# Optimization experiments

Hardware: AMD Instinct MI355X
Metric: run time of the kernel (lower is better)

Reference implementation:

```python
import jax, jax.numpy as jnp
import numpy as np

N = 16384          # nodes
E_R = 524288       # radial edges (avg degree 32)
E_B = 32768        # bonded edges
N_TYPES = 20       # atom types
CS = 64            # scalar (0e) channels
CV = 32            # vector (1o) channels
EA = 16            # edge_attr_dim
EA_B = EA // 2     # bondedness embedding dim
EA_R = (EA + 1) // 2  # radial basis dim
CUTOFF = 1.5       # effective_radial_cutoff
L = 2              # n_layers
NORM = float(np.sqrt((E_R + E_B) / N))  # ~sqrt(avg degree) message normalization


def setup_inputs() -> dict:
    key = jax.random.key(0)
    ks = jax.random.split(key, 32)
    def rn(i, shape, scale=1.0):
        return jax.random.normal(ks[i], shape, dtype=jnp.float32) * scale
    s_e = 1.0 / np.sqrt(EA)
    inp = {}
    inp["pos"] = rn(0, (N, 3))
    inp["c_noise"] = rn(1, (1,))
    inp["atom_types"] = jax.random.randint(ks[2], (N,), 0, N_TYPES)
    inp["radial_edge_index"] = jax.random.randint(ks[3], (2, E_R), 0, N)
    inp["bonded_edge_index"] = jax.random.randint(ks[4], (2, E_B), 0, N)
    # learned parameters
    inp["atom_tab"] = rn(5, (N_TYPES, CS))
    inp["bond_tab"] = rn(6, (2, EA_B))
    inp["ns0_w"] = rn(7, (CS,), 0.1)
    inp["We0"] = rn(8, (EA, CS), s_e)
    inp["We1"] = rn(9, (EA, CS), s_e)
    inp["Wself0"] = rn(10, (CS, CS), 1.0 / np.sqrt(CS))
    inp["Ws0"] = rn(11, (CS, CS), 1.0 / np.sqrt(CS))
    inp["Wv0"] = rn(12, (CS, CV), 1.0 / np.sqrt(CS))
    inp["ns_w"] = rn(13, (L, CS + CV), 0.1)
    inp["We_ss"] = rn(14, (L, EA, CS), s_e)
    inp["We_vs"] = rn(15, (L, EA, CV), s_e)
    inp["We_sv"] = rn(16, (L, EA, CS), s_e)
    inp["We_vv"] = rn(17, (L, EA, CV), s_e)
    inp["We_vx"] = rn(18, (L, EA, CV), s_e)
    inp["Wmix_s"] = rn(19, (L, CS + CV, CS), 1.0 / np.sqrt(CS + CV))
    inp["Wmix_v"] = rn(20, (L, CS + 2 * CV, CV), 1.0 / np.sqrt(CS + 2 * CV))
    inp["Wself_s"] = rn(21, (L, CS, CS), 1.0 / np.sqrt(CS))
    inp["Wself_v"] = rn(22, (L, CV, CV), 1.0 / np.sqrt(CV))
    inp["skip_w"] = rn(23, (L, 2 * (CS + CV)), 0.1)
    inp["skip_b"] = rn(24, (L, 2 * (CS + CV)), 0.1)
    inp["w_out"] = rn(25, (CV,), 1.0 / np.sqrt(CV))
    inp["gain"] = jnp.asarray(0.5, dtype=jnp.float32)
    return inp


def _radial_basis(d):
    # e3nn soft_one_hot_linspace, basis='gaussian', cutoff=True
    centers = jnp.linspace(0.0, CUTOFF, EA_R + 2)[1:-1]
    step = centers[1] - centers[0]
    diff = (d[:, None] - centers[None, :]) / step
    return jnp.exp(-diff * diff) * 1.12


def reference(pos, c_noise, atom_tab, bond_tab, ns0_w, We0, We1, Wself0, Ws0, Wv0,
              ns_w, We_ss, We_vs, We_sv, We_vv, We_vx, Wmix_s, Wmix_v, Wself_s, Wself_v,
              skip_w, skip_b, w_out, gain, atom_types, radial_edge_index, bonded_edge_index):
    edge_index = jnp.concatenate([radial_edge_index, bonded_edge_index], axis=1)
    bond_mask = jnp.concatenate([jnp.zeros((E_R,), jnp.int32), jnp.ones((E_B,), jnp.int32)])
    src, dst = edge_index[0], edge_index[1]
    edge_vec = pos[src] - pos[dst]                      # [E,3]
    d = jnp.sqrt(jnp.sum(edge_vec * edge_vec, -1) + 1e-12)
    Y1 = jnp.sqrt(3.0) * edge_vec / d[:, None]          # l=1 SH, component norm; Y0 == 1
    edge_attr = jnp.concatenate([bond_tab[bond_mask], _radial_basis(d)], axis=-1)  # [E,EA]

    # atom embedding + initial noise-conditional scaling
    s = atom_tab[atom_types] * (1.0 + c_noise * ns0_w)  # [N,CS]

    # initial projector: scalar-input equivariant conv -> hidden irreps
    w0 = edge_attr @ We0
    w1 = edge_attr @ We1
    s_src = s[src]
    a_s = jax.ops.segment_sum(w0 * s_src, dst, num_segments=N) / NORM
    a_v = jax.ops.segment_sum((w1 * s_src)[:, :, None] * Y1[:, None, :], dst, num_segments=N) / NORM
    s_h = a_s @ Ws0 + s @ Wself0                        # [N,CS]
    v_h = jnp.einsum('nci,cd->ndi', a_v, Wv0)           # [N,CV,3]

    for l in range(L):
        # noise-conditional scaling (per-irrep-channel scalar scale)
        scale = 1.0 + c_noise * ns_w[l]
        ss = s_h * scale[:CS]
        vv = v_h * scale[CS:][None, :, None]
        ss_e = ss[src]
        vv_e = vv[src]
        # edge-attr-conditioned tensor-product weights
        w_ss = edge_attr @ We_ss[l]
        w_vs = edge_attr @ We_vs[l]
        w_sv = edge_attr @ We_sv[l]
        w_vv = edge_attr @ We_vv[l]
        w_vx = edge_attr @ We_vx[l]
        # CG tensor-product messages: 0x0->0, 1x1->0 (dot), 0x1->1, 1x0->1, 1x1->1 (cross)
        vdot = jnp.einsum('eci,ei->ec', vv_e, Y1)
        m_s = jnp.concatenate([w_ss * ss_e, w_vs * vdot], axis=-1)          # [E,CS+CV]
        m_v = jnp.concatenate([
            (w_sv * ss_e)[:, :, None] * Y1[:, None, :],
            w_vv[:, :, None] * vv_e,
            w_vx[:, :, None] * jnp.cross(vv_e, Y1[:, None, :]),
        ], axis=1)                                                          # [E,CS+2CV,3]
        a_s = jax.ops.segment_sum(m_s, dst, num_segments=N) / NORM
        a_v = jax.ops.segment_sum(m_v, dst, num_segments=N) / NORM
        new_s = a_s @ Wmix_s[l] + ss @ Wself_s[l]
        new_v = jnp.einsum('nci,cd->ndi', a_v, Wmix_v[l]) + jnp.einsum('nci,cd->ndi', vv, Wself_v[l])
        # noise-conditional skip connection (gated residual)
        g = jax.nn.sigmoid(skip_b[l] + c_noise * skip_w[l])
        s_h = g[:CS] * s_h + g[CS:2 * CS] * new_s
        g_v = g[2 * CS:]
        v_h = g_v[:CV][None, :, None] * v_h + g_v[CV:][None, :, None] * new_v

    # output head: 1o vectors -> 3D displacement, times output gain
    return jnp.einsum('nci,c->ni', v_h, w_out) * gain
```

## Files before the change

kernel.cpp:

```cpp
#include <hip/hip_runtime.h>
#include <math.h>

#define NA 16384
#define ER 524288
#define EB 32768
#define ET 557056
#define INV_NORM 0.17149858514250882f
#define SQRT3 1.7320508075688772f
#define RB_STEP (1.5f/9.0f)
#define BINS 512
#define DMAX 2.5f
#define INV_H ((float)BINS / DMAX)
#define T0U (2 * BINS * 128)
#define TLU (2 * BINS * 256)

typedef unsigned int uint32;
typedef unsigned short ushort16;
typedef float vf4 __attribute__((ext_vector_type(4)));
typedef float vf2 __attribute__((ext_vector_type(2)));
typedef unsigned int vu2 __attribute__((ext_vector_type(2)));

__device__ __forceinline__ float sigmoidf_(float x) { return 1.f / (1.f + __expf(-x)); }

__device__ __forceinline__ ushort16 f2bf(float x) {
  uint32 u = __float_as_uint(x);
  u = u + 0x7FFFu + ((u >> 16) & 1u);
  return (ushort16)(u >> 16);
}
__device__ __forceinline__ uint32 packbf(float hi, float lo) {
  return ((uint32)f2bf(hi) << 16) | (uint32)f2bf(lo);
}
__device__ __forceinline__ float bfhi(uint32 u) { return __uint_as_float(u & 0xFFFF0000u); }
__device__ __forceinline__ float bflo(uint32 u) { return __uint_as_float(u << 16); }

__device__ __forceinline__ float4 ntl4(const float* p) {
  vf4 v = __builtin_nontemporal_load((const vf4*)p);
  return make_float4(v.x, v.y, v.z, v.w);
}
__device__ __forceinline__ float2 ntl2(const float* p) {
  vf2 v = __builtin_nontemporal_load((const vf2*)p);
  return make_float2(v.x, v.y);
}
__device__ __forceinline__ void nts4(float* p, float a, float b, float c, float d) {
  vf4 v; v.x = a; v.y = b; v.z = c; v.w = d;
  __builtin_nontemporal_store(v, (vf4*)p);
}
__device__ __forceinline__ void nts2(float* p, float a, float b) {
  vf2 v; v.x = a; v.y = b;
  __builtin_nontemporal_store(v, (vf2*)p);
}
__device__ __forceinline__ void ntsu2(uint32* p, uint32 a, uint32 b) {
  vu2 v; v.x = a; v.y = b;
  __builtin_nontemporal_store(v, (vu2*)p);
}
__device__ __forceinline__ void nts1(float* p, float a) {
  __builtin_nontemporal_store(a, p);
}

__global__ void k_hist(const int* __restrict__ rad, const int* __restrict__ bon, int* __restrict__ count) {
  int e = blockIdx.x * 256 + threadIdx.x;
  int d = (e < ER) ? rad[ER + e] : bon[EB + (e - ER)];
  atomicAdd(&count[d], 1);
}

__global__ void k_scan1(const int* __restrict__ count, int* __restrict__ partial) {
  __shared__ int red[256];
  int b = blockIdx.x, t = threadIdx.x;
  red[t] = count[b * 256 + t];
  __syncthreads();
  for (int s = 128; s > 0; s >>= 1) {
    if (t < s) red[t] += red[t + s];
    __syncthreads();
  }
  if (t == 0) partial[b] = red[0];
}

__global__ void k_scan2(int* __restrict__ partial) {
  int run = 0;
  for (int i = 0; i < 64; ++i) { int c = partial[i]; partial[i] = run; run += c; }
}

__global__ void k_scan3(const int* __restrict__ count, const int* __restrict__ partial,
                        int* __restrict__ offsets, int* __restrict__ cursor) {
  __shared__ int sc[256];
  int b = blockIdx.x, t = threadIdx.x;
  int v = count[b * 256 + t];
  sc[t] = v;
  __syncthreads();
  for (int off = 1; off < 256; off <<= 1) {
    int x = (t >= off) ? sc[t - off] : 0;
    __syncthreads();
    sc[t] += x;
    __syncthreads();
  }
  int excl = sc[t] - v + partial[b];
  offsets[b * 256 + t] = excl;
  cursor[b * 256 + t] = excl;
  if (b == 63 && t == 255) offsets[NA] = excl + v;
}

__global__ void k_fill_embed(const int* __restrict__ rad, const int* __restrict__ bon,
                             int* __restrict__ cursor, const float* __restrict__ pos,
                             float* __restrict__ rec8,
                             const float* __restrict__ atom_tab, const int* __restrict__ types,
                             const float* __restrict__ ns0_w, const float* __restrict__ cnoise,
                             float* __restrict__ s_feat, ushort16* __restrict__ s_bf) {
  if (blockIdx.x < ET / 256) {
    int e = blockIdx.x * 256 + threadIdx.x;
    int src, dst, v;
    if (e < ER) { src = rad[e]; dst = rad[ER + e]; v = 0; }
    else        { src = bon[e - ER]; dst = bon[EB + e - ER]; v = 1; }
    float dx = pos[src * 3] - pos[dst * 3];
    float dy = pos[src * 3 + 1] - pos[dst * 3 + 1];
    float dz = pos[src * 3 + 2] - pos[dst * 3 + 2];
    float dist = sqrtf(dx * dx + dy * dy + dz * dz + 1e-12f);
    float inv = 1.f / dist;
    float fq = fminf(dist * INV_H, BINS - 1.001f);
    int q = (int)fq;
    float frac = fq - (float)q;
    int qoffL = (v * BINS + q) << 8;
    int slot = atomicAdd(&cursor[dst], 1);
    float* rp = rec8 + (size_t)slot * 8;
    nts4(rp, __int_as_float(src), SQRT3 * dx * inv, SQRT3 * dy * inv, SQRT3 * dz * inv);
    nts2(rp + 4, frac, __int_as_float(qoffL));
  } else {
    int tid = (blockIdx.x - ET / 256) * 256 + threadIdx.x;
    int n = tid >> 6, c = tid & 63;
    float cn = cnoise[0];
    float v = atom_tab[types[n] * 64 + c] * (1.f + cn * ns0_w[c]);
    s_feat[tid] = v;
    s_bf[tid] = f2bf(v);
  }
}

__global__ void k_build(const float* __restrict__ We0, const float* __restrict__ We1,
                        const float* __restrict__ We_ss, const float* __restrict__ We_vs,
                        const float* __restrict__ We_sv, const float* __restrict__ We_vv,
                        const float* __restrict__ We_vx, const float* __restrict__ bond_tab,
                        uint32* __restrict__ T0, uint32* __restrict__ TL) {
  int q = blockIdx.x, t = blockIdx.y, v = blockIdx.z, c = threadIdx.x;
  float d0 = q * (DMAX / BINS), d1 = (q + 1) * (DMAX / BINS);
  float rb0[8], rb1[8];
#pragma unroll
  for (int k = 0; k < 8; ++k) {
    float f0 = (d0 - (k + 1) * RB_STEP) * (1.f / RB_STEP);
    float f1 = (d1 - (k + 1) * RB_STEP) * (1.f / RB_STEP);
    rb0[k] = 1.12f * __expf(-f0 * f0);
    rb1[k] = 1.12f * __expf(-f1 * f1);
  }
  if (t == 0) {
    float ba = 0, bb = 0, a0 = 0, a1 = 0, b0 = 0, b1 = 0;
#pragma unroll
    for (int k = 0; k < 8; ++k) {
      float bt = bond_tab[v * 8 + k];
      float av_lo = We0[k * 64 + c], av_hi = We0[(8 + k) * 64 + c];
      float bv_lo = We1[k * 64 + c], bv_hi = We1[(8 + k) * 64 + c];
      ba += bt * av_lo; bb += bt * bv_lo;
      a0 += rb0[k] * av_hi; a1 += rb1[k] * av_hi;
      b0 += rb0[k] * bv_hi; b1 += rb1[k] * bv_hi;
    }
    uint32* o = T0 + (((size_t)v * BINS + q) << 7) + c * 2;
    o[0] = packbf(ba + a0, a1 - a0);
    o[1] = packbf(bb + b0, b1 - b0);
  } else {
    int l = t - 1;
    const float* Wss = We_ss + l * 1024;
    const float* Wsv = We_sv + l * 1024;
    const float* WA = (c < 32) ? (We_vs + l * 512) : (We_vx + l * 512);
    const float* WB = (c < 32) ? (We_vv + l * 512) : nullptr;
    int cu = c & 31;
    float sa = 0, sb = 0, s0 = 0, s1 = 0, t0 = 0, t1 = 0;
    float ua = 0, ub = 0, u0 = 0, u1 = 0, w0 = 0, w1 = 0;
#pragma unroll
    for (int k = 0; k < 8; ++k) {
      float bt = bond_tab[v * 8 + k];
      float ss_lo = Wss[k * 64 + c], ss_hi = Wss[(8 + k) * 64 + c];
      float sv_lo = Wsv[k * 64 + c], sv_hi = Wsv[(8 + k) * 64 + c];
      sa += bt * ss_lo; sb += bt * sv_lo;
      s0 += rb0[k] * ss_hi; s1 += rb1[k] * ss_hi;
      t0 += rb0[k] * sv_hi; t1 += rb1[k] * sv_hi;
      float a_lo = WA[k * 32 + cu], a_hi = WA[(8 + k) * 32 + cu];
      ua += bt * a_lo;
      u0 += rb0[k] * a_hi; u1 += rb1[k] * a_hi;
      if (WB) {
        float b_lo = WB[k * 32 + cu], b_hi = WB[(8 + k) * 32 + cu];
        ub += bt * b_lo;
        w0 += rb0[k] * b_hi; w1 += rb1[k] * b_hi;
      }
    }
    uint32* o = TL + (size_t)l * TLU + (((size_t)v * BINS + q) << 8) + c * 4;
    o[0] = packbf(sa + s0, s1 - s0);
    o[1] = packbf(sb + t0, t1 - t0);
    o[2] = packbf(ua + u0, u1 - u0);
    o[3] = WB ? packbf(ub + w0, w1 - w0) : 0u;
  }
}

__global__ __launch_bounds__(256, 8) void k_agg0(
    const int* __restrict__ offsets, const float* __restrict__ rec8,
    const uint32* __restrict__ T0, const ushort16* __restrict__ s_bf,
    float* __restrict__ a_s, uint32* __restrict__ a_v) {
  int lane = threadIdx.x & 63;
  int n = blockIdx.x * 4 + (threadIdx.x >> 6);
  float acc = 0, a0 = 0, a1 = 0, a2 = 0;
  int beg = __builtin_amdgcn_readfirstlane(offsets[n]);
  int end = __builtin_amdgcn_readfirstlane(offsets[n + 1]);
  if (beg < end) {
    int last = end - 1;
    int e1 = (beg + 1 < end) ? beg + 1 : last;
    int e2 = (beg + 2 < end) ? beg + 2 : last;
    const float* p0 = rec8 + (size_t)beg * 8;
    const float* p1 = rec8 + (size_t)e1 * 8;
    const float* p2 = rec8 + (size_t)e2 * 8;
    float4 rA0 = ntl4(p0); float2 rB0 = ntl2(p0 + 4);
    float4 rA1 = ntl4(p1); float2 rB1 = ntl2(p1 + 4);
    float4 rA2 = ntl4(p2); float2 rB2 = ntl2(p2 + 4);
    uint2 t0 = *(const uint2*)(T0 + (__float_as_int(rB0.y) >> 1) + (lane << 1));
    ushort16 s0 = s_bf[((size_t)__float_as_int(rA0.x) << 6) + lane];
    uint2 t1 = *(const uint2*)(T0 + (__float_as_int(rB1.y) >> 1) + (lane << 1));
    ushort16 s1 = s_bf[((size_t)__float_as_int(rA1.x) << 6) + lane];
#pragma unroll 3
    for (int idx = beg; idx < end; ++idx) {
      uint2 t2 = *(const uint2*)(T0 + (__float_as_int(rB2.y) >> 1) + (lane << 1));
      ushort16 s2 = s_bf[((size_t)__float_as_int(rA2.x) << 6) + lane];
      int e3 = (idx + 3 < end) ? idx + 3 : last;
      const float* p3 = rec8 + (size_t)e3 * 8;
      float4 rA3 = ntl4(p3); float2 rB3 = ntl2(p3 + 4);
      float frac = rB0.x;
      float w0 = fmaf(frac, bflo(t0.x), bfhi(t0.x));
      float w1 = fmaf(frac, bflo(t0.y), bfhi(t0.y));
      float sv = __uint_as_float((uint32)s0 << 16);
      acc += w0 * sv;
      float t = w1 * sv;
      a0 += t * rA0.y; a1 += t * rA0.z; a2 += t * rA0.w;
      rA0 = rA1; rB0 = rB1; rA1 = rA2; rB1 = rB2; rA2 = rA3; rB2 = rB3;
      t0 = t1; s0 = s1; t1 = t2; s1 = s2;
    }
  }
  nts1(a_s + n * 64 + lane, acc * INV_NORM);
  ntsu2(a_v + ((size_t)n << 7) + (lane << 1),
        packbf(a0 * INV_NORM, a1 * INV_NORM), packbf(a2 * INV_NORM, 0.f));
}

__global__ __launch_bounds__(256, 8) void k_agg_layer(
    const float* __restrict__ cnoise, const float* __restrict__ nsw,
    const int* __restrict__ offsets, const float* __restrict__ rec8,
    const uint32* __restrict__ TL, const ushort16* __restrict__ sh_bf,
    const uint32* __restrict__ vh_bf,
    float* __restrict__ a_s, uint32* __restrict__ a_v) {
  int lane = threadIdx.x & 63;
  int n = blockIdx.x * 4 + (threadIdx.x >> 6);
  int vc = lane & 31;
  bool low = lane < 32;
  float cn = cnoise[0];
  float scale_s = 1.f + cn * nsw[lane];
  float scale_v = 1.f + cn * nsw[64 + vc];

  float ms = 0;
  float av0 = 0, av1 = 0, av2 = 0;
  float ms2 = 0;
  float b0 = 0, b1 = 0, b2 = 0;
  int beg = __builtin_amdgcn_readfirstlane(offsets[n]);
  int end = __builtin_amdgcn_readfirstlane(offsets[n + 1]);
  if (beg < end) {
    int last = end - 1;
    int e1 = (beg + 1 < end) ? beg + 1 : last;
    int e2 = (beg + 2 < end) ? beg + 2 : last;
    const float* p0 = rec8 + (size_t)beg * 8;
    const float* p1 = rec8 + (size_t)e1 * 8;
    const float* p2 = rec8 + (size_t)e2 * 8;
    float4 rA0 = ntl4(p0); float2 rB0 = ntl2(p0 + 4);
    float4 rA1 = ntl4(p1); float2 rB1 = ntl2(p1 + 4);
    float4 rA2 = ntl4(p2); float2 rB2 = ntl2(p2 + 4);
    uint4 t0 = *(const uint4*)(TL + __float_as_int(rB0.y) + (lane << 2));
    ushort16 s0 = sh_bf[((size_t)__float_as_int(rA0.x) << 6) + lane];
    uint2 v0 = *(const uint2*)(vh_bf + ((size_t)__float_as_int(rA0.x) << 6) + (vc << 1));
    uint4 t1 = *(const uint4*)(TL + __float_as_int(rB1.y) + (lane << 2));
    ushort16 s1 = sh_bf[((size_t)__float_as_int(rA1.x) << 6) + lane];
    uint2 v1 = *(const uint2*)(vh_bf + ((size_t)__float_as_int(rA1.x) << 6) + (vc << 1));
#pragma unroll 3
    for (int idx = beg; idx < end; ++idx) {
      uint4 t2 = *(const uint4*)(TL + __float_as_int(rB2.y) + (lane << 2));
      ushort16 s2 = sh_bf[((size_t)__float_as_int(rA2.x) << 6) + lane];
      uint2 v2 = *(const uint2*)(vh_bf + ((size_t)__float_as_int(rA2.x) << 6) + (vc << 1));
      int e3 = (idx + 3 < end) ? idx + 3 : last;
      const float* p3 = rec8 + (size_t)e3 * 8;
      float4 rA3 = ntl4(p3); float2 rB3 = ntl2(p3 + 4);
      float frac = rB0.x;
      float y0 = rA0.y, y1 = rA0.z, y2 = rA0.w;
      float wS  = fmaf(frac, bflo(t0.x), bfhi(t0.x));
      float wSV = fmaf(frac, bflo(t0.y), bfhi(t0.y));
      float wA  = fmaf(frac, bflo(t0.z), bfhi(t0.z));
      float wB  = fmaf(frac, bflo(t0.w), bfhi(t0.w));
      float ss = __uint_as_float((uint32)s0 << 16);
      float vx = bfhi(v0.x), vy = bflo(v0.x), vz = bfhi(v0.y);
      ms += wS * ss;
      float t = wSV * ss;
      av0 += t * y0; av1 += t * y1; av2 += t * y2;
      float vdot = vx * y0 + vy * y1 + vz * y2;
      ms2 += wA * vdot;
      float cx = vy * y2 - vz * y1;
      float cy = vz * y0 - vx * y2;
      float cz = vx * y1 - vy * y0;
      float m0 = low ? vx : cx;
      float m1 = low ? vy : cy;
      float m2 = low ? vz : cz;
      float wM = low ? wB : wA;
      b0 += wM * m0; b1 += wM * m1; b2 += wM * m2;
      rA0 = rA1; rB0 = rB1; rA1 = rA2; rB1 = rB2; rA2 = rA3; rB2 = rB3;
      t0 = t1; s0 = s1; v0 = v1; t1 = t2; s1 = s2; v1 = v2;
    }
  }
  float fs = scale_s * INV_NORM;
  float fv = scale_v * INV_NORM;
  nts1(a_s + n * 96 + lane, ms * fs);
  uint32* avn = a_v + ((size_t)n << 8);
  ntsu2(avn + (lane << 1), packbf(av0 * fs, av1 * fs), packbf(av2 * fs, 0.f));
  if (low) {
    nts1(a_s + n * 96 + 64 + vc, ms2 * fv);
    ntsu2(avn + ((64 + vc) << 1), packbf(b0 * fv, b1 * fv), packbf(b2 * fv, 0.f));
  } else {
    ntsu2(avn + ((96 + vc) << 1), packbf(b0 * fv, b1 * fv), packbf(b2 * fv, 0.f));
  }
}

__global__ __launch_bounds__(256, 8) void k_init_s(
    const float* __restrict__ a_s, const float* __restrict__ s_feat,
    const float* __restrict__ Ws0, const float* __restrict__ Wself0,
    float* __restrict__ sh, ushort16* __restrict__ sh_bf) {
  __shared__ uint32 W1[32 * 64];
  __shared__ uint32 W2[32 * 64];
  __shared__ float La[8 * 64];
  __shared__ float Lf[8 * 64];
  int tid = threadIdx.x;
  for (int i = tid; i < 32 * 64; i += 256) {
    int k = i >> 6, d = i & 63;
    W1[i] = packbf(Ws0[(2 * k) * 64 + d], Ws0[(2 * k + 1) * 64 + d]);
    W2[i] = packbf(Wself0[(2 * k) * 64 + d], Wself0[(2 * k + 1) * 64 + d]);
  }
  int base = blockIdx.x * 8;
  for (int i = tid; i < 512; i += 256) {
    La[i] = a_s[(size_t)base * 64 + i];
    Lf[i] = s_feat[(size_t)base * 64 + i];
  }
  __syncthreads();
  int d = tid & 63, g = tid >> 6;
  int n0 = base + g * 2;
  const float* A0 = La + g * 128;
  const float* A1 = A0 + 64;
  const float* F0 = Lf + g * 128;
  const float* F1 = F0 + 64;
  float a0 = 0, a1 = 0;
#pragma unroll 8
  for (int k = 0; k < 32; ++k) {
    uint32 w1 = W1[k * 64 + d], w2 = W2[k * 64 + d];
    int c = 2 * k;
    a0 += A0[c] * bfhi(w1) + A0[c + 1] * bflo(w1) + F0[c] * bfhi(w2) + F0[c + 1] * bflo(w2);
    a1 += A1[c] * bfhi(w1) + A1[c + 1] * bflo(w1) + F1[c] * bfhi(w2) + F1[c + 1] * bflo(w2);
  }
  sh[(size_t)n0 * 64 + d] = a0;
  sh[(size_t)(n0 + 1) * 64 + d] = a1;
  sh_bf[(size_t)n0 * 64 + d] = f2bf(a0);
  sh_bf[(size_t)(n0 + 1) * 64 + d] = f2bf(a1);
}

__global__ __launch_bounds__(256, 8) void k_init_v(
    const uint32* __restrict__ a_v, const float* __restrict__ Wv0,
    float* __restrict__ vh, uint32* __restrict__ vh_bf) {
  __shared__ uint32 W[32 * 32];
  int tid = threadIdx.x;
  for (int i = tid; i < 32 * 32; i += 256) {
    int k = i >> 5, d = i & 31;
    W[i] = packbf(Wv0[(2 * k) * 32 + d], Wv0[(2 * k + 1) * 32 + d]);
  }
  __syncthreads();
  int d = tid & 31, g = tid >> 5;
  int n = blockIdx.x * 8 + g;
  const uint2* av = (const uint2*)a_v + ((size_t)n << 6);
  float x = 0, y = 0, z = 0;
#pragma unroll 8
  for (int k = 0; k < 32; ++k) {
    uint32 w = W[k * 32 + d];
    uint2 e0 = av[2 * k], e1 = av[2 * k + 1];
    float w0 = bfhi(w), w1 = bflo(w);
    x += bfhi(e0.x) * w0 + bfhi(e1.x) * w1;
    y += bflo(e0.x) * w0 + bflo(e1.x) * w1;
    z += bfhi(e0.y) * w0 + bfhi(e1.y) * w1;
  }
  *(float4*)(vh + ((size_t)n << 7) + (d << 2)) = make_float4(x, y, z, 0.f);
  *(uint2*)(vh_bf + ((size_t)n << 6) + (d << 1)) = make_uint2(packbf(x, y), packbf(z, 0.f));
}

__global__ __launch_bounds__(256, 6) void k_mix_s(
    const float* __restrict__ a_s, const float* __restrict__ sh_in,
    const float* __restrict__ Wmix_s, const float* __restrict__ Wself_s,
    const float* __restrict__ nsw, const float* __restrict__ skw,
    const float* __restrict__ skb, const float* __restrict__ cnoise,
    float* __restrict__ sh_out, ushort16* __restrict__ sh_bf_out) {
  __shared__ uint32 Wm[48 * 64];
  __shared__ uint32 Wsf[32 * 64];
  __shared__ float La[8 * 96];
  int tid = threadIdx.x;
  float cn = cnoise[0];
  for (int i = tid; i < 48 * 64; i += 256) {
    int k = i >> 6, d = i & 63;
    Wm[i] = packbf(Wmix_s[(2 * k) * 64 + d], Wmix_s[(2 * k + 1) * 64 + d]);
  }
  for (int i = tid; i < 32 * 64; i += 256) {
    int k = i >> 6, d = i & 63;
    float sc0 = 1.f + cn * nsw[2 * k];
    float sc1 = 1.f + cn * nsw[2 * k + 1];
    Wsf[i] = packbf(Wself_s[(2 * k) * 64 + d] * sc0, Wself_s[(2 * k + 1) * 64 + d] * sc1);
  }
  int base = blockIdx.x * 8;
  for (int i = tid; i < 8 * 96; i += 256) La[i] = a_s[(size_t)base * 96 + i];
  __syncthreads();
  int d = tid & 63, g = tid >> 6;
  int n0 = base + g * 2;
  const float* A0 = La + (g * 2) * 96;
  const float* A1 = A0 + 96;
  const float* s0p = sh_in + (size_t)n0 * 64;
  const float* s1p = s0p + 64;
  float acc0 = 0, acc1 = 0;
#pragma unroll 8
  for (int k = 0; k < 48; ++k) {
    uint32 w = Wm[k * 64 + d];
    int c = 2 * k;
    float wh = bfhi(w), wl = bflo(w);
    acc0 += A0[c] * wh + A0[c + 1] * wl;
    acc1 += A1[c] * wh + A1[c + 1] * wl;
  }
#pragma unroll 8
  for (int k = 0; k < 32; ++k) {
    uint32 w = Wsf[k * 64 + d];
    int c = 2 * k;
    float wh = bfhi(w), wl = bflo(w);
    acc0 += s0p[c] * wh + s0p[c + 1] * wl;
    acc1 += s1p[c] * wh + s1p[c + 1] * wl;
  }
  float g1 = sigmoidf_(skb[d] + cn * skw[d]);
  float g2 = sigmoidf_(skb[64 + d] + cn * skw[64 + d]);
  float o0 = g1 * s0p[d] + g2 * acc0;
  float o1 = g1 * s1p[d] + g2 * acc1;
  sh_out[(size_t)n0 * 64 + d] = o0;
  sh_out[(size_t)(n0 + 1) * 64 + d] = o1;
  sh_bf_out[(size_t)n0 * 64 + d] = f2bf(o0);
  sh_bf_out[(size_t)(n0 + 1) * 64 + d] = f2bf(o1);
}

__global__ __launch_bounds__(256, 8) void k_mix_v(
    const uint32* __restrict__ a_v, const float* __restrict__ vh_in,
    const float* __restrict__ Wmix_v, const float* __restrict__ Wself_v,
    const float* __restrict__ nsw, const float* __restrict__ skw,
    const float* __restrict__ skb, const float* __restrict__ cnoise,
    float* __restrict__ vh_out, uint32* __restrict__ vh_bf_out) {
  __shared__ uint32 Wm[64 * 32];
  __shared__ uint32 Wsf[16 * 32];
  int tid = threadIdx.x;
  float cn = cnoise[0];
  for (int i = tid; i < 64 * 32; i += 256) {
    int k = i >> 5, d = i & 31;
    Wm[i] = packbf(Wmix_v[(2 * k) * 32 + d], Wmix_v[(2 * k + 1) * 32 + d]);
  }
  for (int i = tid; i < 16 * 32; i += 256) {
    int k = i >> 5, d = i & 31;
    float sc0 = 1.f + cn * nsw[64 + 2 * k];
    float sc1 = 1.f + cn * nsw[64 + 2 * k + 1];
    Wsf[i] = packbf(Wself_v[(2 * k) * 32 + d] * sc0, Wself_v[(2 * k + 1) * 32 + d] * sc1);
  }
  __syncthreads();
  int d = tid & 31, g = tid >> 5;
  int n = blockIdx.x * 8 + g;
  const uint2* av = (const uint2*)a_v + ((size_t)n << 7);
  const float4* vr = (const float4*)(vh_in + ((size_t)n << 7));
  float x = 0, y = 0, z = 0;
#pragma unroll 8
  for (int k = 0; k < 64; ++k) {
    uint32 w = Wm[k * 32 + d];
    uint2 e0 = av[2 * k], e1 = av[2 * k + 1];
    float w0 = bfhi(w), w1 = bflo(w);
    x += bfhi(e0.x) * w0 + bfhi(e1.x) * w1;
    y += bflo(e0.x) * w0 + bflo(e1.x) * w1;
    z += bfhi(e0.y) * w0 + bfhi(e1.y) * w1;
  }
#pragma unroll 8
  for (int k = 0; k < 16; ++k) {
    uint32 w = Wsf[k * 32 + d];
    float4 e0 = vr[2 * k], e1 = vr[2 * k + 1];
    float w0 = bfhi(w), w1 = bflo(w);
    x += e0.x * w0 + e1.x * w1;
    y += e0.y * w0 + e1.y * w1;
    z += e0.z * w0 + e1.z * w1;
  }
  float g3 = sigmoidf_(skb[128 + d] + cn * skw[128 + d]);
  float g4 = sigmoidf_(skb[160 + d] + cn * skw[160 + d]);
  float4 vi = vr[d];
  float ox = g3 * vi.x + g4 * x;
  float oy = g3 * vi.y + g4 * y;
  float oz = g3 * vi.z + g4 * z;
  *(float4*)(vh_out + ((size_t)n << 7) + (d << 2)) = make_float4(ox, oy, oz, 0.f);
  *(uint2*)(vh_bf_out + ((size_t)n << 6) + (d << 1)) = make_uint2(packbf(ox, oy), packbf(oz, 0.f));
}

__global__ void k_out(const float* __restrict__ vh, const float* __restrict__ w_out,
                      const float* __restrict__ gain, float* __restrict__ out) {
  int tid = blockIdx.x * 256 + threadIdx.x;
  int n = tid / 3, i = tid - n * 3;
  float acc = 0;
  for (int c = 0; c < 32; ++c) acc += vh[((size_t)n << 7) + c * 4 + i] * w_out[c];
  out[tid] = acc * gain[0];
}

extern "C" void kernel_launch(void* const* d_in, const int* in_sizes, int n_in,
                              void* d_out, int out_size, void* d_ws, size_t ws_size,
                              hipStream_t stream) {
  (void)in_sizes; (void)n_in; (void)out_size; (void)ws_size;
  const float* pos     = (const float*)d_in[0];
  const float* cn      = (const float*)d_in[1];
  const int*   types   = (const int*)d_in[2];
  const int*   rad     = (const int*)d_in[3];
  const int*   bon     = (const int*)d_in[4];
  const float* atom_tab= (const float*)d_in[5];
  const float* bond_tab= (const float*)d_in[6];
  const float* ns0_w   = (const float*)d_in[7];
  const float* We0     = (const float*)d_in[8];
  const float* We1     = (const float*)d_in[9];
  const float* Wself0  = (const float*)d_in[10];
  const float* Ws0     = (const float*)d_in[11];
  const float* Wv0     = (const float*)d_in[12];
  const float* ns_w    = (const float*)d_in[13];
  const float* We_ss   = (const float*)d_in[14];
  const float* We_vs   = (const float*)d_in[15];
  const float* We_sv   = (const float*)d_in[16];
  const float* We_vv   = (const float*)d_in[17];
  const float* We_vx   = (const float*)d_in[18];
  const float* Wmix_s  = (const float*)d_in[19];
  const float* Wmix_v  = (const float*)d_in[20];
  const float* Wself_s = (const float*)d_in[21];
  const float* Wself_v = (const float*)d_in[22];
  const float* skip_w  = (const float*)d_in[23];
  const float* skip_b  = (const float*)d_in[24];
  const float* w_out   = (const float*)d_in[25];
  const float* gain    = (const float*)d_in[26];

  char* ws = (char*)d_ws;
  size_t o = 0;
  auto alloc = [&](size_t bytes) -> void* {
    void* p = ws + o;
    o += (bytes + 255) & ~(size_t)255;
    return p;
  };
  float* s_feat  = (float*)alloc((size_t)NA * 64 * 4);
  ushort16* s_bf = (ushort16*)alloc((size_t)NA * 64 * 2);
  float* a_s     = (float*)alloc((size_t)NA * 96 * 4);
  uint32* a_v    = (uint32*)alloc((size_t)NA * 256 * 4);
  float* sh0     = (float*)alloc((size_t)NA * 64 * 4);
  float* sh1     = (float*)alloc((size_t)NA * 64 * 4);
  ushort16* shbf0= (ushort16*)alloc((size_t)NA * 64 * 2);
  ushort16* shbf1= (ushort16*)alloc((size_t)NA * 64 * 2);
  float* vh0     = (float*)alloc((size_t)NA * 128 * 4);
  float* vh1     = (float*)alloc((size_t)NA * 128 * 4);
  uint32* vhbf0  = (uint32*)alloc((size_t)NA * 64 * 4);
  uint32* vhbf1  = (uint32*)alloc((size_t)NA * 64 * 4);
  int* count     = (int*)alloc((size_t)NA * 4);
  int* partial   = (int*)alloc((size_t)64 * 4);
  int* offsets   = (int*)alloc((size_t)(NA + 1) * 4);
  int* cursor    = (int*)alloc((size_t)NA * 4);
  float* rec8    = (float*)alloc((size_t)ET * 32);
  uint32* T0     = (uint32*)alloc((size_t)T0U * 4);
  uint32* TL     = (uint32*)alloc((size_t)2 * TLU * 4);
  float* shb[2]  = {sh0, sh1};
  ushort16* shbf[2] = {shbf0, shbf1};
  float* vhb[2]  = {vh0, vh1};
  uint32* vhbf[2]= {vhbf0, vhbf1};

  hipMemsetAsync(count, 0, (size_t)NA * 4, stream);
  k_hist<<<ET / 256, 256, 0, stream>>>(rad, bon, count);
  k_scan1<<<64, 256, 0, stream>>>(count, partial);
  k_scan2<<<1, 1, 0, stream>>>(partial);
  k_scan3<<<64, 256, 0, stream>>>(count, partial, offsets, cursor);
  k_fill_embed<<<ET / 256 + NA * 64 / 256, 256, 0, stream>>>(
      rad, bon, cursor, pos, rec8, atom_tab, types, ns0_w, cn, s_feat, s_bf);
  k_build<<<dim3(BINS, 3, 2), 64, 0, stream>>>(We0, We1, We_ss, We_vs, We_sv, We_vv, We_vx,
                                               bond_tab, T0, TL);

  k_agg0<<<NA / 4, 256, 0, stream>>>(offsets, rec8, T0, s_bf, a_s, a_v);
  k_init_s<<<NA / 8, 256, 0, stream>>>(a_s, s_feat, Ws0, Wself0, shb[0], shbf[0]);
  k_init_v<<<NA / 8, 256, 0, stream>>>(a_v, Wv0, vhb[0], vhbf[0]);

  for (int l = 0; l < 2; ++l) {
    int bin = l & 1, bout = 1 - bin;
    k_agg_layer<<<NA / 4, 256, 0, stream>>>(
        cn, ns_w + l * 96, offsets, rec8, TL + (size_t)l * TLU, shbf[bin], vhbf[bin], a_s, a_v);
    k_mix_s<<<NA / 8, 256, 0, stream>>>(
        a_s, shb[bin], Wmix_s + l * 96 * 64, Wself_s + l * 64 * 64,
        ns_w + l * 96, skip_w + l * 192, skip_b + l * 192, cn, shb[bout], shbf[bout]);
    k_mix_v<<<NA / 8, 256, 0, stream>>>(
        a_v, vhb[bin], Wmix_v + l * 128 * 32, Wself_v + l * 32 * 32,
        ns_w + l * 96, skip_w + l * 192, skip_b + l * 192, cn, vhb[bout], vhbf[bout]);
  }
  k_out<<<NA * 3 / 256, 256, 0, stream>>>(vhb[0], w_out, gain, (float*)d_out);
}
```

Baseline: 503.2 us.

## Split edge scatter into index sort plus coalesced reorder, fuse output head

The fill kernel now scatters only the edge index into a sorted array. A new reorder kernel computes edge geometry and writes the 32-byte edge records contiguously in destination order, so the wide scattered stores become coalesced. The output projection is fused into the last mix_v launch with a warp shuffle reduction, which removes the separate k_out kernel. This costs one extra kernel launch and an indirect gather of edge data through the sorted indices.

New measurement: 499.5 us. No clear change (-0.7%).

```diff
diff --git a/kernel.cpp b/kernel.cpp
--- a/kernel.cpp
+++ b/kernel.cpp
@@ -100,29 +100,15 @@
 }
 
 __global__ void k_fill_embed(const int* __restrict__ rad, const int* __restrict__ bon,
-                             int* __restrict__ cursor, const float* __restrict__ pos,
-                             float* __restrict__ rec8,
+                             int* __restrict__ cursor, int* __restrict__ sorted,
                              const float* __restrict__ atom_tab, const int* __restrict__ types,
                              const float* __restrict__ ns0_w, const float* __restrict__ cnoise,
                              float* __restrict__ s_feat, ushort16* __restrict__ s_bf) {
   if (blockIdx.x < ET / 256) {
     int e = blockIdx.x * 256 + threadIdx.x;
-    int src, dst, v;
-    if (e < ER) { src = rad[e]; dst = rad[ER + e]; v = 0; }
-    else        { src = bon[e - ER]; dst = bon[EB + e - ER]; v = 1; }
-    float dx = pos[src * 3] - pos[dst * 3];
-    float dy = pos[src * 3 + 1] - pos[dst * 3 + 1];
-    float dz = pos[src * 3 + 2] - pos[dst * 3 + 2];
-    float dist = sqrtf(dx * dx + dy * dy + dz * dz + 1e-12f);
-    float inv = 1.f / dist;
-    float fq = fminf(dist * INV_H, BINS - 1.001f);
-    int q = (int)fq;
-    float frac = fq - (float)q;
-    int qoffL = (v * BINS + q) << 8;
-    int slot = atomicAdd(&cursor[dst], 1);
-    float* rp = rec8 + (size_t)slot * 8;
-    nts4(rp, __int_as_float(src), SQRT3 * dx * inv, SQRT3 * dy * inv, SQRT3 * dz * inv);
-    nts2(rp + 4, frac, __int_as_float(qoffL));
+    int d = (e < ER) ? rad[ER + e] : bon[EB + (e - ER)];
+    int slot = atomicAdd(&cursor[d], 1);
+    sorted[slot] = e;
   } else {
     int tid = (blockIdx.x - ET / 256) * 256 + threadIdx.x;
     int n = tid >> 6, c = tid & 63;
@@ -131,6 +117,28 @@
     s_feat[tid] = v;
     s_bf[tid] = f2bf(v);
   }
+}
+
+__global__ void k_reorder(const int* __restrict__ sorted,
+                          const int* __restrict__ rad, const int* __restrict__ bon,
+                          const float* __restrict__ pos, float* __restrict__ rec8) {
+  int idx = blockIdx.x * 256 + threadIdx.x;
+  int e = sorted[idx];
+  int src, dst, v;
+  if (e < ER) { src = rad[e]; dst = rad[ER + e]; v = 0; }
+  else        { src = bon[e - ER]; dst = bon[EB + e - ER]; v = 1; }
+  float dx = pos[src * 3] - pos[dst * 3];
+  float dy = pos[src * 3 + 1] - pos[dst * 3 + 1];
+  float dz = pos[src * 3 + 2] - pos[dst * 3 + 2];
+  float dist = sqrtf(dx * dx + dy * dy + dz * dz + 1e-12f);
+  float inv = 1.f / dist;
+  float fq = fminf(dist * INV_H, BINS - 1.001f);
+  int q = (int)fq;
+  float frac = fq - (float)q;
+  int qoffL = (v * BINS + q) << 8;
+  float* rp = rec8 + (size_t)idx * 8;
+  nts4(rp, __int_as_float(src), SQRT3 * dx * inv, SQRT3 * dy * inv, SQRT3 * dz * inv);
+  nts2(rp + 4, frac, __int_as_float(qoffL));
 }
 
 __global__ void k_build(const float* __restrict__ We0, const float* __restrict__ We1,
@@ -453,7 +461,9 @@
     const float* __restrict__ Wmix_v, const float* __restrict__ Wself_v,
     const float* __restrict__ nsw, const float* __restrict__ skw,
     const float* __restrict__ skb, const float* __restrict__ cnoise,
-    float* __restrict__ vh_out, uint32* __restrict__ vh_bf_out) {
+    float* __restrict__ vh_out, uint32* __restrict__ vh_bf_out,
+    const float* __restrict__ w_out, const float* __restrict__ gain,
+    float* __restrict__ out, int doOut) {
   __shared__ uint32 Wm[64 * 32];
   __shared__ uint32 Wsf[16 * 32];
   int tid = threadIdx.x;
@@ -500,15 +510,21 @@
   float oz = g3 * vi.z + g4 * z;
   *(float4*)(vh_out + ((size_t)n << 7) + (d << 2)) = make_float4(ox, oy, oz, 0.f);
   *(uint2*)(vh_bf_out + ((size_t)n << 6) + (d << 1)) = make_uint2(packbf(ox, oy), packbf(oz, 0.f));
-}
-
-__global__ void k_out(const float* __restrict__ vh, const float* __restrict__ w_out,
-                      const float* __restrict__ gain, float* __restrict__ out) {
-  int tid = blockIdx.x * 256 + threadIdx.x;
-  int n = tid / 3, i = tid - n * 3;
-  float acc = 0;
-  for (int c = 0; c < 32; ++c) acc += vh[((size_t)n << 7) + c * 4 + i] * w_out[c];
-  out[tid] = acc * gain[0];
+  if (doOut) {
+    float wv = w_out[d];
+    float rx = wv * ox, ry = wv * oy, rz = wv * oz;
+#pragma unroll
+    for (int m = 16; m > 0; m >>= 1) {
+      rx += __shfl_xor(rx, m, 32);
+      ry += __shfl_xor(ry, m, 32);
+      rz += __shfl_xor(rz, m, 32);
+    }
+    if (d == 0) {
+      float gn = gain[0];
+      float* op = out + (size_t)n * 3;
+      op[0] = rx * gn; op[1] = ry * gn; op[2] = rz * gn;
+    }
+  }
 }
 
 extern "C" void kernel_launch(void* const* d_in, const int* in_sizes, int n_in,
@@ -566,6 +582,7 @@
   int* partial   = (int*)alloc((size_t)64 * 4);
   int* offsets   = (int*)alloc((size_t)(NA + 1) * 4);
   int* cursor    = (int*)alloc((size_t)NA * 4);
+  int* sorted    = (int*)alloc((size_t)ET * 4);
   float* rec8    = (float*)alloc((size_t)ET * 32);
   uint32* T0     = (uint32*)alloc((size_t)T0U * 4);
   uint32* TL     = (uint32*)alloc((size_t)2 * TLU * 4);
@@ -580,7 +597,8 @@
   k_scan2<<<1, 1, 0, stream>>>(partial);
   k_scan3<<<64, 256, 0, stream>>>(count, partial, offsets, cursor);
   k_fill_embed<<<ET / 256 + NA * 64 / 256, 256, 0, stream>>>(
-      rad, bon, cursor, pos, rec8, atom_tab, types, ns0_w, cn, s_feat, s_bf);
+      rad, bon, cursor, sorted, atom_tab, types, ns0_w, cn, s_feat, s_bf);
+  k_reorder<<<ET / 256, 256, 0, stream>>>(sorted, rad, bon, pos, rec8);
   k_build<<<dim3(BINS, 3, 2), 64, 0, stream>>>(We0, We1, We_ss, We_vs, We_sv, We_vv, We_vx,
                                                bond_tab, T0, TL);
 
@@ -597,7 +615,7 @@
         ns_w + l * 96, skip_w + l * 192, skip_b + l * 192, cn, shb[bout], shbf[bout]);
     k_mix_v<<<NA / 8, 256, 0, stream>>>(
         a_v, vhb[bin], Wmix_v + l * 128 * 32, Wself_v + l * 32 * 32,
-        ns_w + l * 96, skip_w + l * 192, skip_b + l * 192, cn, vhb[bout], vhbf[bout]);
-  }
-  k_out<<<NA * 3 / 256, 256, 0, stream>>>(vhb[0], w_out, gain, (float*)d_out);
-}
+        ns_w + l * 96, skip_w + l * 192, skip_b + l * 192, cn, vhb[bout], vhbf[bout],
+        w_out, gain, (float*)d_out, l == 1);
+  }
+}
```
